# Kernel tuning notes

Measured on AMD Instinct MI355X. Metric: run time of the kernel, lower is better.

The kernel has to match this reference:

```python
import jax, jax.numpy as jnp
import numpy as np


def setup_inputs() -> dict:
    key = jax.random.key(0)
    ks = jax.random.split(key, 6)
    B = 16
    return {
        "concat_gap": jax.random.normal(ks[0], (B, 448), dtype=jnp.float32),
        "out1": jax.random.normal(ks[1], (B, 64, 15, 64, 64), dtype=jnp.float32),
        "out2": jax.random.normal(ks[2], (B, 128, 8, 32, 32), dtype=jnp.float32),
        "out3": jax.random.normal(ks[3], (B, 256, 4, 16, 16), dtype=jnp.float32),
        "weight": jax.random.normal(ks[4], (3, 448), dtype=jnp.float32) * 0.05,
        "bias": jax.random.normal(ks[5], (3,), dtype=jnp.float32) * 0.05,
    }


def _vis(out, w_covid, w_cap):
    # fused channel-wise weighted reduction: (sum_c out[:,c]*w0[c] + sum_c out[:,c]*w1[c]) / 2
    w = (w_covid + w_cap) * 0.5  # [C]
    v = jnp.einsum('bcdhw,c->bdhw', out, w)
    return v[:, None]  # [B,1,D,H,W]


def reference(concat_gap, out1, out2, out3, weight, bias):
    # fc_out = addmm(bias, concat_gap, weight.T)
    fc_out = concat_gap @ weight.T + bias  # [B,3]
    vis1 = _vis(out1, weight[0, :64], weight[1, :64])
    vis2 = _vis(out2, weight[0, 64:192], weight[1, 64:192])
    vis3 = _vis(out3, weight[0, 192:448], weight[1, 192:448])
    return (fc_out, vis1, vis2, vis3)
```

## Files before the change

kernel.cpp:

```cpp
#include <hip/hip_runtime.h>


#define VIS3_BLOCKS 16
#define VIS2_BLOCKS 128
#define VIS1_BLOCKS 960
#define TOTAL_BLOCKS (VIS3_BLOCKS + VIS2_BLOCKS + VIS1_BLOCKS + 1)

__global__ __launch_bounds__(256) void fused_vis_fc_kernel(
    const float* __restrict__ concat_gap,
    const float* __restrict__ out1,
    const float* __restrict__ out2,
    const float* __restrict__ out3,
    const float* __restrict__ weight,
    const float* __restrict__ bias,
    float* __restrict__ d_out)
{
    const int t = threadIdx.x;
    int blk = blockIdx.x;

    const float* in;
    float* out;
    int C, bpb, woff;

    if (blk < VIS3_BLOCKS) {
        in = out3; out = d_out + 48 + 983040 + 131072;
        C = 256; bpb = 1; woff = 192;
    } else if (blk < VIS3_BLOCKS + VIS2_BLOCKS) {
        blk -= VIS3_BLOCKS;
        in = out2; out = d_out + 48 + 983040;
        C = 128; bpb = 8; woff = 64;
    } else if (blk < VIS3_BLOCKS + VIS2_BLOCKS + VIS1_BLOCKS) {
        blk -= VIS3_BLOCKS + VIS2_BLOCKS;
        in = out1; out = d_out + 48;
        C = 64; bpb = 60; woff = 0;
    } else {
        if (t < 48) {
            const int b = t / 3, o = t % 3;
            const float* g = concat_gap + b * 448;
            const float* w = weight + o * 448;
            float s = 0.f;
            #pragma unroll 8
            for (int k = 0; k < 448; ++k) s += g[k] * w[k];
            d_out[t] = s + bias[o];
        }
        return;
    }

    __shared__ float s_w[256];
    for (int c = t; c < C; c += 256)
        s_w[c] = 0.5f * (weight[woff + c] + weight[448 + woff + c]);
    __syncthreads();

    const int b  = blk / bpb;
    const int s4 = (blk % bpb) * 256 + t;
    const int S4 = bpb * 256;

    const float4* in4 = (const float4*)in + (size_t)b * C * S4 + s4;

    float4 acc = make_float4(0.f, 0.f, 0.f, 0.f);
    #pragma unroll 8
    for (int c = 0; c < C; ++c) {
        float4 v = in4[(size_t)c * S4];
        const float w = s_w[c];
        acc.x += v.x * w;
        acc.y += v.y * w;
        acc.z += v.z * w;
        acc.w += v.w * w;
    }
    ((float4*)out)[(size_t)b * S4 + s4] = acc;
}

extern "C" void kernel_launch(void* const* d_in, const int* in_sizes, int n_in,
                              void* d_out, int out_size, void* d_ws, size_t ws_size,
                              hipStream_t stream) {
    const float* concat_gap = (const float*)d_in[0];
    const float* out1       = (const float*)d_in[1];
    const float* out2       = (const float*)d_in[2];
    const float* out3       = (const float*)d_in[3];
    const float* weight     = (const float*)d_in[4];
    const float* bias       = (const float*)d_in[5];
    float* out              = (float*)d_out;

    fused_vis_fc_kernel<<<TOTAL_BLOCKS, 256, 0, stream>>>(
        concat_gap, out1, out2, out3, weight, bias, out);
}
```

Measured before the change: 409.8 us.

## Rebalance vis block partition and use nontemporal vector loads/stores

```diff
diff --git a/kernel.cpp b/kernel.cpp
--- a/kernel.cpp
+++ b/kernel.cpp
@@ -1,12 +1,16 @@
 #include <hip/hip_runtime.h>
 
 
-#define VIS3_BLOCKS 16
-#define VIS2_BLOCKS 128
-#define VIS1_BLOCKS 960
-#define TOTAL_BLOCKS (VIS3_BLOCKS + VIS2_BLOCKS + VIS1_BLOCKS + 1)
+typedef float fvec4 __attribute__((ext_vector_type(4)));
 
-__global__ __launch_bounds__(256) void fused_vis_fc_kernel(
+__device__ __forceinline__ fvec4 ntload(const fvec4* p) {
+    return __builtin_nontemporal_load(p);
+}
+__device__ __forceinline__ void ntstore(fvec4* p, fvec4 v) {
+    __builtin_nontemporal_store(v, p);
+}
+
+__global__ __launch_bounds__(256) void fused_vis_fc_v2(
     const float* __restrict__ concat_gap,
     const float* __restrict__ out1,
     const float* __restrict__ out2,
@@ -18,21 +22,65 @@
     const int t = threadIdx.x;
     int blk = blockIdx.x;
 
-    const float* in;
-    float* out;
-    int C, bpb, woff;
+    __shared__ float s_w[256];
+    __shared__ fvec4 s_red[128];
 
-    if (blk < VIS3_BLOCKS) {
-        in = out3; out = d_out + 48 + 983040 + 131072;
-        C = 256; bpb = 1; woff = 192;
-    } else if (blk < VIS3_BLOCKS + VIS2_BLOCKS) {
-        blk -= VIS3_BLOCKS;
-        in = out2; out = d_out + 48 + 983040;
-        C = 128; bpb = 8; woff = 64;
-    } else if (blk < VIS3_BLOCKS + VIS2_BLOCKS + VIS1_BLOCKS) {
-        blk -= VIS3_BLOCKS + VIS2_BLOCKS;
-        in = out1; out = d_out + 48;
-        C = 64; bpb = 60; woff = 0;
+    if (blk < 32) {
+        const int b    = blk >> 1;
+        const int s4   = ((blk & 1) << 7) + (t & 127);
+        const int half = t >> 7;
+        for (int c = t; c < 256; c += 256)
+            s_w[c] = 0.5f * (weight[192 + c] + weight[640 + c]);
+        __syncthreads();
+
+        const fvec4* in4 = (const fvec4*)out3
+            + (size_t)b * 256 * 256 + (size_t)(half * 128) * 256 + s4;
+        fvec4 acc = {0.f, 0.f, 0.f, 0.f};
+        #pragma unroll 8
+        for (int c = 0; c < 128; ++c)
+            acc += ntload(in4 + (size_t)c * 256) * s_w[half * 128 + c];
+
+        if (half) s_red[t & 127] = acc;
+        __syncthreads();
+        if (!half) {
+            acc += s_red[t];
+            ntstore((fvec4*)(d_out + 48 + 983040 + 131072) + b * 256 + s4, acc);
+        }
+    } else if (blk < 160) {
+        blk -= 32;
+        const int b  = blk >> 3;
+        const int s4 = ((blk & 7) << 8) + t;
+        for (int c = t; c < 128; c += 256)
+            s_w[c] = 0.5f * (weight[64 + c] + weight[512 + c]);
+        __syncthreads();
+
+        const fvec4* in4 = (const fvec4*)out2 + (size_t)b * 128 * 2048 + s4;
+        fvec4 acc = {0.f, 0.f, 0.f, 0.f};
+        #pragma unroll 8
+        for (int c = 0; c < 128; ++c)
+            acc += ntload(in4 + (size_t)c * 2048) * s_w[c];
+        ntstore((fvec4*)(d_out + 48 + 983040) + b * 2048 + s4, acc);
+    } else if (blk < 640) {
+        blk -= 160;
+        const int b     = blk / 30;
+        const int chunk = (blk % 30) * 512;
+        for (int c = t; c < 64; c += 256)
+            s_w[c] = 0.5f * (weight[c] + weight[448 + c]);
+        __syncthreads();
+
+        const fvec4* in4 = (const fvec4*)out1
+            + (size_t)b * 64 * 15360 + chunk + t;
+        fvec4 a0 = {0.f, 0.f, 0.f, 0.f};
+        fvec4 a1 = {0.f, 0.f, 0.f, 0.f};
+        #pragma unroll 8
+        for (int c = 0; c < 64; ++c) {
+            const float w = s_w[c];
+            a0 += ntload(in4 + (size_t)c * 15360) * w;
+            a1 += ntload(in4 + (size_t)c * 15360 + 256) * w;
+        }
+        fvec4* o = (fvec4*)(d_out + 48) + (size_t)b * 15360 + chunk + t;
+        ntstore(o, a0);
+        ntstore(o + 256, a1);
     } else {
         if (t < 48) {
             const int b = t / 3, o = t % 3;
@@ -43,44 +91,14 @@
             for (int k = 0; k < 448; ++k) s += g[k] * w[k];
             d_out[t] = s + bias[o];
         }
-        return;
     }
-
-    __shared__ float s_w[256];
-    for (int c = t; c < C; c += 256)
-        s_w[c] = 0.5f * (weight[woff + c] + weight[448 + woff + c]);
-    __syncthreads();
-
-    const int b  = blk / bpb;
-    const int s4 = (blk % bpb) * 256 + t;
-    const int S4 = bpb * 256;
-
-    const float4* in4 = (const float4*)in + (size_t)b * C * S4 + s4;
-
-    float4 acc = make_float4(0.f, 0.f, 0.f, 0.f);
-    #pragma unroll 8
-    for (int c = 0; c < C; ++c) {
-        float4 v = in4[(size_t)c * S4];
-        const float w = s_w[c];
-        acc.x += v.x * w;
-        acc.y += v.y * w;
-        acc.z += v.z * w;
-        acc.w += v.w * w;
-    }
-    ((float4*)out)[(size_t)b * S4 + s4] = acc;
 }
 
 extern "C" void kernel_launch(void* const* d_in, const int* in_sizes, int n_in,
                               void* d_out, int out_size, void* d_ws, size_t ws_size,
                               hipStream_t stream) {
-    const float* concat_gap = (const float*)d_in[0];
-    const float* out1       = (const float*)d_in[1];
-    const float* out2       = (const float*)d_in[2];
-    const float* out3       = (const float*)d_in[3];
-    const float* weight     = (const float*)d_in[4];
-    const float* bias       = (const float*)d_in[5];
-    float* out              = (float*)d_out;
-
-    fused_vis_fc_kernel<<<TOTAL_BLOCKS, 256, 0, stream>>>(
-        concat_gap, out1, out2, out3, weight, bias, out);
+    fused_vis_fc_v2<<<641, 256, 0, stream>>>(
+        (const float*)d_in[0], (const float*)d_in[1], (const float*)d_in[2],
+        (const float*)d_in[3], (const float*)d_in[4], (const float*)d_in[5],
+        (float*)d_out);
 }
```

Result: faster. 370.4 us (-9.6%).
